# Kernel tuning notes

Measured on AMD Instinct MI355X. Metric: run time of the kernel, lower is better.

Reference implementation:

```python
import jax, jax.numpy as jnp
import numpy as np

B, S, H, G, W_LOC = 2, 4096, 12, 64, 513  # Longformer-base: window=2*256+1, 64 global slots


def setup_inputs() -> dict:
    key = jax.random.key(0)
    k1, = jax.random.split(key, 1)
    attention_probs = jax.random.uniform(k1, (B, S, H, G + W_LOC), dtype=jnp.float32)
    attention_mask = jnp.zeros((B, S), dtype=jnp.float32)  # all tokens currently kept
    # global tokens are the first G positions of every batch; nonzero(as_tuple) index arrays
    b_idx = jnp.repeat(jnp.arange(B, dtype=jnp.int64), G)
    g_idx = jnp.tile(jnp.arange(G, dtype=jnp.int64), B)
    return {
        "attention_mask": attention_mask,
        "attention_probs": attention_probs,
        "keep_threshold": jnp.asarray(0.005, dtype=jnp.float32),  # base 0.01*6/12 + learned 0
        "max_num_global_attn_indices": G,
        "loc_b": b_idx, "loc_i": g_idx,
        "glob_b": b_idx, "glob_i": g_idx,
    }


def reference(attention_mask, attention_probs, keep_threshold,
              max_num_global_attn_indices, loc_b, loc_i, glob_b, glob_i):
    Gn = max_num_global_attn_indices
    b, s, h, wg = attention_probs.shape
    w = wg - Gn  # local window size, odd
    half = w // 2

    # zero out rows of already-masked tokens (attention_mask < 0)
    probs = jnp.where((attention_mask < 0)[:, :, None, None], 0.0, attention_probs)

    gl = probs[..., :Gn]                              # [B,S,H,G]
    lo = jnp.transpose(probs[..., Gn:], (0, 2, 1, 3))  # [B,H,S,W]

    # anti-diagonal (key-column) sums of the local band; equals the source's
    # conv2d-with-flipped-identity + slice: out[j] = sum_c lo[j + half - c, c]
    lo_p = jnp.pad(lo, ((0, 0), (0, 0), (half, half), (0, 0)))  # [B,H,S+W-1,W]
    rows = jnp.arange(s)[:, None] + (w - 1) - jnp.arange(w)[None, :]  # [S,W]
    diag = lo_p[:, :, rows, jnp.arange(w)[None, :]]  # [B,H,S,W]
    local_sum = diag.sum(axis=(1, 3))                # [B,S] (summed over heads too)

    global_sum = gl.sum(axis=(1, 2))                 # [B,G]
    probs_sum = local_sum.at[loc_b, loc_i].add(global_sum[glob_b, glob_i])

    probs_max = probs_sum.max(axis=-1, keepdims=True)
    scores = probs_sum / probs_max

    thr = jnp.maximum(jnp.float32(1e-5), jnp.asarray(keep_threshold, jnp.float32).reshape(()))
    new_attention_mask = jnp.where(scores < thr, jnp.float32(-10000.0), jnp.float32(0.0))
    return new_attention_mask, scores
```

## Files before the change

### kernel.cpp

```cpp
#include <hip/hip_runtime.h>
#include <float.h>

#define Bsz 2
#define Ssz 4096
#define Hsz 12
#define Gsz 64
#define Wsz 513
#define Csz (Gsz + Wsz)
#define ROW (Hsz * Csz)
#define HALF 256

#define COLSUM_OFF  0
#define COLSUM_SZ   ((size_t)Bsz * Ssz * Wsz)
#define PSUM_OFF    COLSUM_SZ
#define PSUM_SZ     ((size_t)Bsz * Ssz)
#define GACC_OFF    (PSUM_OFF + PSUM_SZ)
#define GACC_SZ     ((size_t)Bsz * Gsz)

__global__ __launch_bounds__(256) void k1_rowsum(
    const float* __restrict__ probs, const float* __restrict__ mask,
    float* __restrict__ colsum, float* __restrict__ gacc)
{
    __shared__ float lds[ROW];
    const int t = threadIdx.x;
    const int row0 = blockIdx.x * 8;
    const int b = row0 / Ssz;
    float g = 0.f;

    for (int r = 0; r < 8; ++r) {
        const int row = row0 + r;
        const float4* src = (const float4*)(probs + (size_t)row * ROW);
        float4* dst = (float4*)lds;
        for (int idx = t; idx < ROW / 4; idx += 256) dst[idx] = src[idx];
        __syncthreads();

        const float scale = (mask[row] < 0.f) ? 0.f : 1.f;
        const int s = row - b * Ssz;
        for (int c = t; c < Csz; c += 256) {
            float v = 0.f;
            #pragma unroll
            for (int h = 0; h < Hsz; ++h) v += lds[h * Csz + c];
            v *= scale;
            if (c < Gsz) g += v;
            else colsum[((size_t)b * Ssz + s) * Wsz + (c - Gsz)] = v;
        }
        __syncthreads();
    }
    if (t < Gsz) atomicAdd(&gacc[b * Gsz + t], g);
}

__global__ __launch_bounds__(256) void k2_diag(
    const float* __restrict__ colsum, float* __restrict__ psum)
{
    const int t  = threadIdx.x;
    const int i0 = blockIdx.y * 256;
    const int b  = blockIdx.z;
    const int i  = i0 + t;
    int s_begin = i0 - 256 + (int)blockIdx.x * 256;
    int s_end   = s_begin + 256;
    if (s_begin < 0) s_begin = 0;
    if (s_end > Ssz) s_end = Ssz;

    const float* base = colsum + (size_t)b * Ssz * Wsz + (i + HALF);
    float acc = 0.f;
    for (int s = s_begin; s < s_end; ++s) {
        int j = i + HALF - s;
        if (j >= 0 && j < Wsz) acc += base[(size_t)s * (Wsz - 1)];
    }
    atomicAdd(&psum[b * Ssz + i], acc);
}

__global__ void k3_scatter(const int* __restrict__ loc_b, const int* __restrict__ loc_i,
                           const int* __restrict__ glob_b, const int* __restrict__ glob_i,
                           const float* __restrict__ gacc, float* __restrict__ psum, int n)
{
    int k = blockIdx.x * blockDim.x + threadIdx.x;
    if (k < n)
        atomicAdd(&psum[loc_b[k] * Ssz + loc_i[k]], gacc[glob_b[k] * Gsz + glob_i[k]]);
}

__global__ __launch_bounds__(1024) void k4_final(
    const float* __restrict__ psum, const float* __restrict__ thr_p,
    float* __restrict__ out)
{
    const int b = blockIdx.x;
    const int t = threadIdx.x;
    const float* p = psum + (size_t)b * Ssz;

    float m = -FLT_MAX;
    for (int i = t; i < Ssz; i += 1024) m = fmaxf(m, p[i]);
    #pragma unroll
    for (int off = 32; off >= 1; off >>= 1) m = fmaxf(m, __shfl_down(m, off, 64));

    __shared__ float red[16];
    const int wave = t >> 6, lane = t & 63;
    if (lane == 0) red[wave] = m;
    __syncthreads();
    if (t == 0) {
        float mm = red[0];
        #pragma unroll
        for (int w = 1; w < 16; ++w) mm = fmaxf(mm, red[w]);
        red[0] = mm;
    }
    __syncthreads();
    const float mx = red[0];
    const float thr = fmaxf(1e-5f, thr_p[0]);

    for (int i = t; i < Ssz; i += 1024) {
        float sc = p[i] / mx;
        out[(size_t)Bsz * Ssz + (size_t)b * Ssz + i] = sc;
        out[(size_t)b * Ssz + i] = (sc < thr) ? -10000.f : 0.f;
    }
}

extern "C" void kernel_launch(void* const* d_in, const int* in_sizes, int n_in,
                              void* d_out, int out_size, void* d_ws, size_t ws_size,
                              hipStream_t stream)
{
    const float* mask  = (const float*)d_in[0];
    const float* probs = (const float*)d_in[1];
    const float* thr   = (const float*)d_in[2];
    const int* loc_b  = (const int*)d_in[4];
    const int* loc_i  = (const int*)d_in[5];
    const int* glob_b = (const int*)d_in[6];
    const int* glob_i = (const int*)d_in[7];
    const int n_idx = in_sizes[4];

    float* ws     = (float*)d_ws;
    float* colsum = ws + COLSUM_OFF;
    float* psum   = ws + PSUM_OFF;
    float* gacc   = ws + GACC_OFF;
    float* out    = (float*)d_out;

    hipMemsetAsync(psum, 0, (PSUM_SZ + GACC_SZ) * sizeof(float), stream);

    k1_rowsum<<<dim3(Bsz * Ssz / 8), dim3(256), 0, stream>>>(probs, mask, colsum, gacc);
    k2_diag<<<dim3(3, Ssz / 256, Bsz), dim3(256), 0, stream>>>(colsum, psum);
    k3_scatter<<<dim3(1), dim3(128), 0, stream>>>(loc_b, loc_i, glob_b, glob_i, gacc, psum, n_idx);
    k4_final<<<dim3(Bsz), dim3(1024), 0, stream>>>(psum, thr, out);
}
```

Before: 404.6 us.

## Fuse anti-diagonal band sum into row-sum kernel via shared-memory window

```diff
diff --git a/kernel.cpp b/kernel.cpp
--- a/kernel.cpp
+++ b/kernel.cpp
@@ -9,65 +9,51 @@
 #define Csz (Gsz + Wsz)
 #define ROW (Hsz * Csz)
 #define HALF 256
+#define RPB 8
+#define WIN (RPB + Wsz - 1)
 
-#define COLSUM_OFF  0
-#define COLSUM_SZ   ((size_t)Bsz * Ssz * Wsz)
-#define PSUM_OFF    COLSUM_SZ
-#define PSUM_SZ     ((size_t)Bsz * Ssz)
-#define GACC_OFF    (PSUM_OFF + PSUM_SZ)
-#define GACC_SZ     ((size_t)Bsz * Gsz)
+#define PSUM_SZ ((size_t)Bsz * Ssz)
+#define GACC_SZ ((size_t)Bsz * Gsz)
 
-__global__ __launch_bounds__(256) void k1_rowsum(
+__global__ __launch_bounds__(256) void k1_fused(
     const float* __restrict__ probs, const float* __restrict__ mask,
-    float* __restrict__ colsum, float* __restrict__ gacc)
+    float* __restrict__ psum, float* __restrict__ gacc)
 {
     __shared__ float lds[ROW];
+    __shared__ float win[WIN];
     const int t = threadIdx.x;
-    const int row0 = blockIdx.x * 8;
+    const int row0 = blockIdx.x * RPB;
     const int b = row0 / Ssz;
     float g = 0.f;
 
-    for (int r = 0; r < 8; ++r) {
+    for (int w = t; w < WIN; w += 256) win[w] = 0.f;
+
+    for (int r = 0; r < RPB; ++r) {
         const int row = row0 + r;
         const float4* src = (const float4*)(probs + (size_t)row * ROW);
         float4* dst = (float4*)lds;
+        #pragma unroll
         for (int idx = t; idx < ROW / 4; idx += 256) dst[idx] = src[idx];
         __syncthreads();
 
         const float scale = (mask[row] < 0.f) ? 0.f : 1.f;
-        const int s = row - b * Ssz;
         for (int c = t; c < Csz; c += 256) {
             float v = 0.f;
             #pragma unroll
             for (int h = 0; h < Hsz; ++h) v += lds[h * Csz + c];
             v *= scale;
             if (c < Gsz) g += v;
-            else colsum[((size_t)b * Ssz + s) * Wsz + (c - Gsz)] = v;
+            else win[r + (c - Gsz)] += v;
         }
         __syncthreads();
     }
+
+    const int i_base = (row0 - b * Ssz) - HALF;
+    for (int w = t; w < WIN; w += 256) {
+        const int i = i_base + w;
+        if (i >= 0 && i < Ssz) atomicAdd(&psum[b * Ssz + i], win[w]);
+    }
     if (t < Gsz) atomicAdd(&gacc[b * Gsz + t], g);
-}
-
-__global__ __launch_bounds__(256) void k2_diag(
-    const float* __restrict__ colsum, float* __restrict__ psum)
-{
-    const int t  = threadIdx.x;
-    const int i0 = blockIdx.y * 256;
-    const int b  = blockIdx.z;
-    const int i  = i0 + t;
-    int s_begin = i0 - 256 + (int)blockIdx.x * 256;
-    int s_end   = s_begin + 256;
-    if (s_begin < 0) s_begin = 0;
-    if (s_end > Ssz) s_end = Ssz;
-
-    const float* base = colsum + (size_t)b * Ssz * Wsz + (i + HALF);
-    float acc = 0.f;
-    for (int s = s_begin; s < s_end; ++s) {
-        int j = i + HALF - s;
-        if (j >= 0 && j < Wsz) acc += base[(size_t)s * (Wsz - 1)];
-    }
-    atomicAdd(&psum[b * Ssz + i], acc);
 }
 
 __global__ void k3_scatter(const int* __restrict__ loc_b, const int* __restrict__ loc_i,
@@ -126,16 +112,13 @@
     const int* glob_i = (const int*)d_in[7];
     const int n_idx = in_sizes[4];
 
-    float* ws     = (float*)d_ws;
-    float* colsum = ws + COLSUM_OFF;
-    float* psum   = ws + PSUM_OFF;
-    float* gacc   = ws + GACC_OFF;
-    float* out    = (float*)d_out;
+    float* psum = (float*)d_ws;
+    float* gacc = psum + PSUM_SZ;
+    float* out  = (float*)d_out;
 
     hipMemsetAsync(psum, 0, (PSUM_SZ + GACC_SZ) * sizeof(float), stream);
 
-    k1_rowsum<<<dim3(Bsz * Ssz / 8), dim3(256), 0, stream>>>(probs, mask, colsum, gacc);
-    k2_diag<<<dim3(3, Ssz / 256, Bsz), dim3(256), 0, stream>>>(colsum, psum);
+    k1_fused<<<dim3(Bsz * Ssz / RPB), dim3(256), 0, stream>>>(probs, mask, psum, gacc);
     k3_scatter<<<dim3(1), dim3(128), 0, stream>>>(loc_b, loc_i, glob_b, glob_i, gacc, psum, n_idx);
     k4_final<<<dim3(Bsz), dim3(1024), 0, stream>>>(psum, thr, out);
 }
```

New measurement: 332.6 us. -17.8%, faster.
